# Performance work log

Hardware: AMD Instinct MI355X
Metric: run time of the kernel (lower is better)

The kernel has to match this reference:

```python
import jax, jax.numpy as jnp
import numpy as np

N, DEG, D_FEAT, D_OUT = 50000, 32, 128, 256

def setup_inputs() -> dict:
    key = jax.random.key(0)
    k1, k2, k3 = jax.random.split(key, 3)
    features = jax.random.normal(k1, (N, D_FEAT), dtype=jnp.float32)
    edge_look_up = jax.random.randint(k2, (N, DEG), 0, N, dtype=jnp.int64)
    # glorot-uniform kernel, shape (2*D_FEAT, D_OUT)
    limit = np.sqrt(6.0 / (2 * D_FEAT + D_OUT)).astype(np.float32)
    kernel = jax.random.uniform(k3, (2 * D_FEAT, D_OUT), dtype=jnp.float32,
                                minval=-limit, maxval=limit)
    return {"features": features, "edge_look_up": edge_look_up, "kernel": kernel}

def reference(features, edge_look_up, kernel):
    # [1] neighborhood aggregation: gather neighbor features and mean-reduce
    neigh = features[edge_look_up]          # [N, DEG, D_FEAT] (irregular gather)
    agg = jnp.mean(neigh, axis=1)           # [N, D_FEAT]
    # [2] concat self features with aggregated neighbor vectors
    out = jnp.concatenate([features, agg], axis=-1)  # [N, 2*D_FEAT]
    # [4] dense matmul + [5] relu activation
    return jax.nn.relu(out @ kernel)        # [N, D_OUT]
```

## Files before the change

### kernel.cpp

```cpp
#include <hip/hip_runtime.h>

#define NN  50000
#define DEG 32
#define DF  128
#define DO  256
#define FEAT4 (NN * DF / 4)

typedef __bf16 bf16x8 __attribute__((ext_vector_type(8)));
typedef float  f32x4  __attribute__((ext_vector_type(4)));
typedef float  f32x2  __attribute__((ext_vector_type(2)));
typedef unsigned short u16x8 __attribute__((ext_vector_type(8)));

#if defined(__has_builtin)
#if __has_builtin(__builtin_amdgcn_cvt_pk_f32_fp8) && __has_builtin(__builtin_amdgcn_cvt_pk_fp8_f32)
#define HW_FP8 1
#endif
#endif
#ifndef HW_FP8
#define HW_FP8 0
#endif

__device__ __forceinline__ unsigned short f2bf(float f) {
    unsigned u = __float_as_uint(f);
    u += 0x7FFF + ((u >> 16) & 1);
    return (unsigned short)(u >> 16);
}

#if !HW_FP8
__device__ __forceinline__ unsigned enc1_fp8(float f) {
    unsigned u = __float_as_uint(f);
    unsigned s = (u >> 31) << 7;
    float a = fabsf(f);
    if (!(a > 0.f)) return s;
    if (a >= 448.f) return s | 0x7E;
    u = __float_as_uint(a);
    int e = (int)((u >> 23) & 255) - 127;
    if (e < -6) {
        unsigned m = (unsigned)(a * 512.f + 0.5f);
        if (m >= 8) return s | 0x08;
        return s | m;
    }
    unsigned mant = (u >> 20) & 7;
    unsigned rnd  = ((u >> 19) & 1) & (((u & 0x7FFFF) != 0) | ((u >> 20) & 1));
    unsigned enc  = ((unsigned)(e + 7) << 3) | mant;
    return s | (enc + rnd);
}
__device__ __forceinline__ float dec1_fp8(unsigned b) {
    unsigned s = (b >> 7) & 1, e = (b >> 3) & 15, m = b & 7;
    float v = (e == 0) ? (float)m * 0.001953125f
                       : __uint_as_float(((e - 7 + 127) << 23) | (m << 20));
    return s ? -v : v;
}
#endif

__device__ __forceinline__ unsigned enc4_fp8(float4 v) {
#if HW_FP8
    int pk = 0;
    pk = __builtin_amdgcn_cvt_pk_fp8_f32(v.x, v.y, pk, false);
    pk = __builtin_amdgcn_cvt_pk_fp8_f32(v.z, v.w, pk, true);
    return (unsigned)pk;
#else
    return enc1_fp8(v.x) | (enc1_fp8(v.y) << 8) | (enc1_fp8(v.z) << 16) | (enc1_fp8(v.w) << 24);
#endif
}

__global__ __launch_bounds__(256) void convert_kernel(
    const float* __restrict__ feat, const float* __restrict__ W,
    unsigned* __restrict__ feat8, unsigned short* __restrict__ featb,
    unsigned short* __restrict__ Wt)
{
    const int gid = blockIdx.x * 256 + threadIdx.x;
    if (gid < FEAT4) {
        const float4 v = ((const float4*)feat)[gid];
        feat8[gid] = enc4_fp8(v);
        ushort4 o;
        o.x = f2bf(v.x); o.y = f2bf(v.y); o.z = f2bf(v.z); o.w = f2bf(v.w);
        ((ushort4*)featb)[gid] = o;
    } else {
        const int t = gid - FEAT4;
        if (t < DO * DO) {
            const int n = t >> 8, k = t & 255;
            Wt[n * DO + k] = f2bf(W[k * DO + n]);
        }
    }
}

__global__ __launch_bounds__(256) void agg_kernel(
    const unsigned* __restrict__ feat8,
    const int*      __restrict__ edges,
    unsigned short* __restrict__ aggb)
{
    const int node = blockIdx.x * 16 + (threadIdx.x >> 4);
    const int l    = threadIdx.x & 15;
    const int* e   = edges + node * DEG;

    float a[8] = {0.f, 0.f, 0.f, 0.f, 0.f, 0.f, 0.f, 0.f};
    #pragma unroll
    for (int d = 0; d < DEG; ++d) {
        const int idx = e[d];
        const uint2 pk = *(const uint2*)(feat8 + (size_t)idx * (DF / 4) + l * 2);
#if HW_FP8
        const f32x2 v0 = __builtin_amdgcn_cvt_pk_f32_fp8((int)pk.x, false);
        const f32x2 v1 = __builtin_amdgcn_cvt_pk_f32_fp8((int)pk.x, true);
        const f32x2 v2 = __builtin_amdgcn_cvt_pk_f32_fp8((int)pk.y, false);
        const f32x2 v3 = __builtin_amdgcn_cvt_pk_f32_fp8((int)pk.y, true);
        a[0] += v0[0]; a[1] += v0[1]; a[2] += v1[0]; a[3] += v1[1];
        a[4] += v2[0]; a[5] += v2[1]; a[6] += v3[0]; a[7] += v3[1];
#else
        #pragma unroll
        for (int j = 0; j < 4; ++j) a[j]     += dec1_fp8((pk.x >> (8 * j)) & 255);
        #pragma unroll
        for (int j = 0; j < 4; ++j) a[4 + j] += dec1_fp8((pk.y >> (8 * j)) & 255);
#endif
    }

    const float s = 1.0f / (float)DEG;
    u16x8 o;
    #pragma unroll
    for (int j = 0; j < 8; ++j) o[j] = f2bf(a[j] * s);
    *(u16x8*)(aggb + (size_t)node * DF + l * 8) = o;
}

#define BM 64

__global__ __launch_bounds__(256) void gemm_kernel(
    const unsigned short* __restrict__ featb,
    const unsigned short* __restrict__ aggb,
    const unsigned short* __restrict__ Wt,
    float*                __restrict__ out)
{
    const int tid  = threadIdx.x;
    const int m0   = blockIdx.x * BM;
    const int wave = tid >> 6, lane = tid & 63;
    const int quad = lane >> 4, lr = lane & 15;
    const int wn   = wave * 64;

    f32x4 acc[4][4] = {};

    #pragma unroll
    for (int kk = 0; kk < 256; kk += 32) {
        const unsigned short* Asrc = (kk < DF) ? (featb + kk) : (aggb + (kk - DF));
        bf16x8 af[4], bfr[4];
        #pragma unroll
        for (int i = 0; i < 4; ++i) {
            int row = m0 + i * 16 + lr;
            if (row >= NN) row = NN - 1;
            af[i]  = *(const bf16x8*)(Asrc + (size_t)row * DF + quad * 8);
            bfr[i] = *(const bf16x8*)(Wt + (size_t)(wn + i * 16 + lr) * DO + kk + quad * 8);
        }
        #pragma unroll
        for (int mi = 0; mi < 4; ++mi)
            #pragma unroll
            for (int ni = 0; ni < 4; ++ni)
                acc[mi][ni] = __builtin_amdgcn_mfma_f32_16x16x32_bf16(
                    af[mi], bfr[ni], acc[mi][ni], 0, 0, 0);
    }

    #pragma unroll
    for (int mi = 0; mi < 4; ++mi) {
        #pragma unroll
        for (int r = 0; r < 4; ++r) {
            const int row = m0 + mi * 16 + quad * 4 + r;
            if (row < NN) {
                #pragma unroll
                for (int ni = 0; ni < 4; ++ni) {
                    out[(size_t)row * DO + wn + ni * 16 + lr] =
                        fmaxf(acc[mi][ni][r], 0.f);
                }
            }
        }
    }
}

extern "C" void kernel_launch(void* const* d_in, const int* in_sizes, int n_in,
                              void* d_out, int out_size, void* d_ws, size_t ws_size,
                              hipStream_t stream)
{
    const float* feat  = (const float*)d_in[0];
    const int*   edges = (const int*)d_in[1];
    const float* W     = (const float*)d_in[2];
    float*       out   = (float*)d_out;

    unsigned short* aggb  = (unsigned short*)d_ws;
    unsigned*       feat8 = (unsigned*)(aggb + (size_t)NN * DF);
    unsigned short* featb = (unsigned short*)(feat8 + (size_t)NN * DF / 4);
    unsigned short* Wt    = featb + (size_t)NN * DF;

    convert_kernel<<<(FEAT4 + DO * DO + 255) / 256, 256, 0, stream>>>(
        feat, W, feat8, featb, Wt);
    agg_kernel<<<NN / 16, 256, 0, stream>>>(feat8, edges, aggb);
    gemm_kernel<<<(NN + BM - 1) / BM, 256, 0, stream>>>(featb, aggb, Wt, out);
}
```

Measured before the change: 144.2 us.

## Stage GEMM A/B tiles in LDS with 128x128 block tiling

Reworks the GEMM to stage 128x64 chunks of the activation and weight matrices in padded shared memory and have each of four waves compute a 64x64 quadrant. A 2D grid splits the output columns in two. This is meant to cut redundant global loads of A fragments that every wave previously issued on its own. In exchange it adds two barriers per k-chunk and single-buffered LDS staging with no overlap of loads and compute.

```diff
diff --git a/kernel.cpp b/kernel.cpp
--- a/kernel.cpp
+++ b/kernel.cpp
@@ -121,7 +121,9 @@
     *(u16x8*)(aggb + (size_t)node * DF + l * 8) = o;
 }
 
-#define BM 64
+#define BM  128
+#define BN  128
+#define LDA 72
 
 __global__ __launch_bounds__(256) void gemm_kernel(
     const unsigned short* __restrict__ featb,
@@ -129,42 +131,66 @@
     const unsigned short* __restrict__ Wt,
     float*                __restrict__ out)
 {
+    __shared__ __align__(16) unsigned short Asw[BM * LDA];
+    __shared__ __align__(16) unsigned short Bsw[BN * LDA];
+
     const int tid  = threadIdx.x;
     const int m0   = blockIdx.x * BM;
+    const int c0   = blockIdx.y * BN;
     const int wave = tid >> 6, lane = tid & 63;
     const int quad = lane >> 4, lr = lane & 15;
-    const int wn   = wave * 64;
+    const int wm   = (wave & 1) * 64;
+    const int wn   = (wave >> 1) * 64;
+
+    const int srow = tid >> 3;
+    const int sseg = (tid & 7) * 8;
 
     f32x4 acc[4][4] = {};
 
-    #pragma unroll
-    for (int kk = 0; kk < 256; kk += 32) {
-        const unsigned short* Asrc = (kk < DF) ? (featb + kk) : (aggb + (kk - DF));
-        bf16x8 af[4], bfr[4];
-        #pragma unroll
-        for (int i = 0; i < 4; ++i) {
-            int row = m0 + i * 16 + lr;
-            if (row >= NN) row = NN - 1;
-            af[i]  = *(const bf16x8*)(Asrc + (size_t)row * DF + quad * 8);
-            bfr[i] = *(const bf16x8*)(Wt + (size_t)(wn + i * 16 + lr) * DO + kk + quad * 8);
-        }
-        #pragma unroll
-        for (int mi = 0; mi < 4; ++mi)
+    for (int kc = 0; kc < 4; ++kc) {
+        const unsigned short* srcA = (kc < 2) ? (featb + kc * 64)
+                                              : (aggb + (kc - 2) * 64);
+        const unsigned short* srcB = Wt + kc * 64;
+
+        __syncthreads();
+        #pragma unroll
+        for (int p = 0; p < 4; ++p) {
+            const int r = p * 32 + srow;
+            int node = m0 + r;
+            if (node >= NN) node = NN - 1;
+            const float4 va = *(const float4*)(srcA + (size_t)node * DF + sseg);
+            *(float4*)(Asw + r * LDA + sseg) = va;
+            const float4 vb = *(const float4*)(srcB + (size_t)(c0 + r) * DO + sseg);
+            *(float4*)(Bsw + r * LDA + sseg) = vb;
+        }
+        __syncthreads();
+
+        #pragma unroll
+        for (int kk = 0; kk < 64; kk += 32) {
+            bf16x8 af[4], bfr[4];
             #pragma unroll
-            for (int ni = 0; ni < 4; ++ni)
-                acc[mi][ni] = __builtin_amdgcn_mfma_f32_16x16x32_bf16(
-                    af[mi], bfr[ni], acc[mi][ni], 0, 0, 0);
+            for (int i = 0; i < 4; ++i) {
+                af[i]  = *(const bf16x8*)(Asw + (wm + i * 16 + lr) * LDA + kk + quad * 8);
+                bfr[i] = *(const bf16x8*)(Bsw + (wn + i * 16 + lr) * LDA + kk + quad * 8);
+            }
+            #pragma unroll
+            for (int mi = 0; mi < 4; ++mi)
+                #pragma unroll
+                for (int ni = 0; ni < 4; ++ni)
+                    acc[mi][ni] = __builtin_amdgcn_mfma_f32_16x16x32_bf16(
+                        af[mi], bfr[ni], acc[mi][ni], 0, 0, 0);
+        }
     }
 
     #pragma unroll
     for (int mi = 0; mi < 4; ++mi) {
         #pragma unroll
         for (int r = 0; r < 4; ++r) {
-            const int row = m0 + mi * 16 + quad * 4 + r;
+            const int row = m0 + wm + mi * 16 + quad * 4 + r;
             if (row < NN) {
                 #pragma unroll
                 for (int ni = 0; ni < 4; ++ni) {
-                    out[(size_t)row * DO + wn + ni * 16 + lr] =
+                    out[(size_t)row * DO + c0 + wn + ni * 16 + lr] =
                         fmaxf(acc[mi][ni][r], 0.f);
                 }
             }
@@ -189,5 +215,7 @@
     convert_kernel<<<(FEAT4 + DO * DO + 255) / 256, 256, 0, stream>>>(
         feat, W, feat8, featb, Wt);
     agg_kernel<<<NN / 16, 256, 0, stream>>>(feat8, edges, aggb);
-    gemm_kernel<<<(NN + BM - 1) / BM, 256, 0, stream>>>(featb, aggb, Wt, out);
-}
+
+    dim3 grid((NN + BM - 1) / BM, DO / BN);
+    gemm_kernel<<<grid, 256, 0, stream>>>(featb, aggb, Wt, out);
+}
```

New measurement: 123.0 us (median of 2 runs). 14.7% less time.
